# Kernel tuning notes

Measured on AMD Instinct MI355X. Metric: run time of the kernel, lower is better.

The kernel has to match this reference:

```python
import jax, jax.numpy as jnp
import numpy as np

B, T, F, H = 32, 1024, 128, 256
NUM_LAYERS = 3  # 2 return_sequences LSTMs + final LSTM


def setup_inputs() -> dict:
    key = jax.random.key(0)
    ks = jax.random.split(key, 2 + 3 * NUM_LAYERS + 2)
    x = jax.random.normal(ks[0], (B, 2, T, F), jnp.float32)
    # ragged lengths: pad tail with zeros (Masking(mask_value=0) semantics)
    lengths = jax.random.randint(ks[1], (B, 2), T // 4, T + 1)
    tmask = (jnp.arange(T)[None, None, :] < lengths[:, :, None]).astype(jnp.float32)
    x = x * tmask[..., None]
    inp = {"inputs": x}
    in_dims = [F] + [H] * (NUM_LAYERS - 1)
    for i, d in enumerate(in_dims):
        k = 2 + 3 * i
        inp[f"W{i}"] = jax.random.normal(ks[k], (d, 4 * H), jnp.float32) * (1.0 / np.sqrt(d))
        inp[f"U{i}"] = jax.random.normal(ks[k + 1], (H, 4 * H), jnp.float32) * (1.0 / np.sqrt(H))
        b = jnp.zeros((4 * H,), jnp.float32)
        inp[f"b{i}"] = b.at[H:2 * H].set(1.0)  # keras unit_forget_bias
    inp["dense_w"] = jax.random.normal(ks[-2], (1, 1), jnp.float32)
    inp["dense_b"] = jnp.zeros((1,), jnp.float32)
    return inp


def lstm_layer(x, mask, W, U, b):
    """Keras-style masked LSTM. x: [B,T,D], mask: [B,T] bool.
    Masked steps carry previous h/c and previous output (keras K.rnn masking).
    Gate order i,f,g,o; sigmoid recurrent activation, tanh activation."""
    xT = jnp.swapaxes(x, 0, 1)                  # [T,B,D]
    mT = jnp.swapaxes(mask, 0, 1)[..., None]    # [T,B,1]
    bsz, hd = x.shape[0], U.shape[0]
    h0 = jnp.zeros((bsz, hd), x.dtype)

    def step(carry, inp):
        h, c = carry
        x_t, m = inp
        z = x_t @ W + h @ U + b                 # [B,4H]
        i, f, g, o = jnp.split(z, 4, axis=-1)
        c_new = jax.nn.sigmoid(f) * c + jax.nn.sigmoid(i) * jnp.tanh(g)
        h_new = jax.nn.sigmoid(o) * jnp.tanh(c_new)
        h = jnp.where(m, h_new, h)
        c = jnp.where(m, c_new, c)
        return (h, c), h

    (h_final, _), ys = jax.lax.scan(step, (h0, h0), (xT, mT))
    return jnp.swapaxes(ys, 0, 1), h_final


def encode(x, Ws, Us, bs):
    mask = jnp.any(x != 0, axis=-1)             # Masking(mask_value=0)
    for W, U, b in zip(Ws[:-1], Us[:-1], bs[:-1]):
        x, _ = lstm_layer(x, mask, W, U, b)     # dropout is identity at inference
    _, h = lstm_layer(x, mask, Ws[-1], Us[-1], bs[-1])
    return h


def reference(inputs, W0, U0, b0, W1, U1, b1, W2, U2, b2, dense_w, dense_b):
    Ws, Us, bs = [W0, W1, W2], [U0, U1, U2], [b0, b1, b2]
    h1 = encode(inputs[:, 0], Ws, Us, bs)
    h2 = encode(inputs[:, 1], Ws, Us, bs)
    dist = jnp.linalg.norm(h1 - h2, axis=1, keepdims=True)   # [B,1]
    dist = jnp.clip(dist, 1e-7, 1e7)
    return jax.nn.sigmoid(dist @ dense_w + dense_b)          # [B,1]
```

## Files before the change

### kernel.cpp

```cpp
#include <hip/hip_runtime.h>


typedef __attribute__((ext_vector_type(8))) short bf16x8;
typedef __attribute__((ext_vector_type(4))) float f32x4;
typedef __attribute__((ext_vector_type(4))) unsigned int u32x4;
typedef unsigned long long ull;

__device__ __forceinline__ unsigned short f2bf(float f){
    unsigned u = __float_as_uint(f);
    u += 0x7FFFu + ((u >> 16) & 1u);
    return (unsigned short)(u >> 16);
}
__device__ __forceinline__ float fsig(float x){ return 1.0f / (1.0f + __expf(-x)); }
__device__ __forceinline__ float ftanh(float x){
    float e = __expf(-2.0f * fabsf(x));
    float t = (1.0f - e) / (1.0f + e);
    return copysignf(t, x);
}
__device__ __forceinline__ ull ald(const ull* p){
    return __hip_atomic_load(p, __ATOMIC_RELAXED, __HIP_MEMORY_SCOPE_AGENT);
}
__device__ __forceinline__ void ast(unsigned int* p, unsigned int v){
    __hip_atomic_store(p, v, __ATOMIC_RELAXED, __HIP_MEMORY_SCOPE_AGENT);
}
__device__ __forceinline__ int min4(ull a, ull b){
    int x0 = (int)(unsigned)a, x1 = (int)(a >> 32);
    int x2 = (int)(unsigned)b, x3 = (int)(b >> 32);
    return min(min(x0, x1), min(x2, x3));
}

#define LOAD4_SC1(P, O0,O1,O2,O3)                                        \
  asm volatile("global_load_dwordx4 %0, %4, off sc1\n\t"                 \
               "global_load_dwordx4 %1, %4, off offset:1024 sc1\n\t"     \
               "global_load_dwordx4 %2, %4, off offset:2048 sc1\n\t"     \
               "global_load_dwordx4 %3, %4, off offset:3072 sc1"         \
               : "=&v"(O0),"=&v"(O1),"=&v"(O2),"=&v"(O3)                 \
               : "v"(P) : "memory")
#define LOAD4_PLAIN(P, O0,O1,O2,O3)                                      \
  asm volatile("global_load_dwordx4 %0, %4, off\n\t"                     \
               "global_load_dwordx4 %1, %4, off offset:1024\n\t"         \
               "global_load_dwordx4 %2, %4, off offset:2048\n\t"         \
               "global_load_dwordx4 %3, %4, off offset:3072"             \
               : "=&v"(O0),"=&v"(O1),"=&v"(O2),"=&v"(O3)                 \
               : "v"(P) : "memory")

__global__ void prep_kernel(const float* __restrict__ x, unsigned int* __restrict__ xb,
                            unsigned int* __restrict__ mb, int* __restrict__ fl){
    const int s = blockIdx.x, c = blockIdx.y, l = threadIdx.x;
    if (s == 0 && c == 0){ for (int i = l; i < 256; i += 64) fl[i] = 0; }
    const int g = s >> 4, sg = s & 15;
    const int woff = ((l >> 4) * 4 + ((l >> 2) & 3)) * 64 + sg * 4 + (l & 3);
    const float* xs = x + ((size_t)s * 1024 + (size_t)c * 64) * 128;
    unsigned int w0 = 0, w1 = 0;
    for (int tt = 0; tt < 64; ++tt){
        const float2 v = *(const float2*)(xs + (size_t)tt * 128 + 2 * l);
        bool nz = (v.x != 0.0f) || (v.y != 0.0f);
        unsigned long long b = __ballot(nz);
        if (b){ if (tt < 32) w0 |= 1u << tt; else w1 |= 1u << (tt - 32); }
        unsigned int p = (unsigned)f2bf(v.x) | ((unsigned)f2bf(v.y) << 16);
        xb[((size_t)(c * 64 + tt) * 4 + g) * 1024 + woff] = p;
    }
    if (l == 0){ mb[s * 32 + c * 2] = w0; mb[s * 32 + c * 2 + 1] = w1; }
}

template<int LAYER>
__device__ __forceinline__ void scan_layer(
    const unsigned int* xin,
    unsigned int* hout,
    const float* __restrict__ W, const float* __restrict__ U, const float* __restrict__ Bv,
    const unsigned int* __restrict__ mb,
    float* __restrict__ hfinal,
    int* flags)
{
    constexpr int DK = (LAYER == 0) ? 4 : 8;
    constexpr int KT = DK + 8;
    const int bid = blockIdx.x & 15;
    const int g = bid >> 2, n = bid & 3;
    const int tid  = threadIdx.x;
    const int w    = tid >> 6;
    const int lane = tid & 63;
    const int l15  = lane & 15, lk = lane >> 4;
    const int up   = lane & 7,  s2 = lane >> 3;

    __shared__ float zw[4][16][68];
    __shared__ unsigned int mbL[16][32];
    __shared__ int sgl;
    if (tid == 0) sgl = 0;
    for (int i = tid; i < 512; i += 256)
        mbL[i >> 5][i & 31] = mb[(g * 16 + (i >> 5)) * 32 + (i & 31)];
    __syncthreads();
    if (tid < 16){
        int last = 0;
        #pragma unroll
        for (int q = 0; q < 32; ++q){
            unsigned v = mbL[tid][q];
            if (v) last = q * 32 + (32 - __clz(v));
        }
        atomicMax(&sgl, last);
    }

    float bfr[4]; int gcol[4];
    #pragma unroll
    for (int nt = 0; nt < 4; ++nt){
        int lc = w * 64 + nt * 16 + l15;
        gcol[nt] = (lc & 3) * 256 + n * 64 + (lc >> 2);
        bfr[nt] = Bv[gcol[nt]];
    }
    bf16x8 Bf[KT][4];
    #pragma unroll
    for (int kt = 0; kt < KT; ++kt){
        const float* src = (kt < DK) ? (W + (size_t)(kt * 32 + lk * 8) * 1024)
                                     : (U + (size_t)((kt - DK) * 32 + lk * 8) * 1024);
        #pragma unroll
        for (int nt = 0; nt < 4; ++nt){
            bf16x8 v;
            #pragma unroll
            for (int j = 0; j < 8; ++j) v[j] = (short)f2bf(src[(size_t)j * 1024 + gcol[nt]]);
            Bf[kt][nt] = v;
        }
    }
    __syncthreads();
    const int gl = sgl;
    int* pF  = flags + (LAYER * 4 + g) * 16;
    int* pG  = flags + ((LAYER > 0 ? LAYER - 1 : 0) * 4 + g) * 16;

    float c00 = 0, c01 = 0, c10 = 0, c11 = 0;
    float h00 = 0, h01 = 0, h10 = 0, h11 = 0;
    const int myseq0 = g * 16 + s2, myseq1 = g * 16 + s2 + 8;
    const int hcol = n * 32 + w * 8 + up;
    const int woff0 = ((hcol >> 4) * 4 + ((hcol >> 2) & 3)) * 64 + s2 * 4 + (hcol & 3);

    for (int t = 0; t < gl; ++t){
        u32x4 x0v,x1v,x2v,x3v,x4v,x5v,x6v,x7v;
        u32x4 h0v,h1v,h2v,h3v,h4v,h5v,h6v,h7v;
        if (LAYER == 0){
            ull xaddr = (ull)((const char*)(xin + ((size_t)t * 4 + g) * 1024) + lane * 16);
            LOAD4_PLAIN(xaddr, x0v, x1v, x2v, x3v);
        }
        if (LAYER > 0 || t > 0){
            const ull* f  = (const ull*)pF;
            const ull* gq = (const ull*)pG;
            int spins = 0;
            for (;;){
                bool ok = true;
                if (t > 0)           ok = (min4(ald(f),  ald(f + 1))  >= t);
                if (LAYER > 0 && ok) ok = (min4(ald(gq), ald(gq + 1)) >= t + 1);
                if (ok) break;
                if ((++spins & 63) == 0) __builtin_amdgcn_s_sleep(1);
            }
        }
        if (LAYER > 0){
            ull xaddr = (ull)((const char*)(xin + ((size_t)t * 4 + g) * 2048) + lane * 16);
            LOAD4_SC1(xaddr,        x0v, x1v, x2v, x3v);
            LOAD4_SC1(xaddr + 4096, x4v, x5v, x6v, x7v);
        }
        if (t > 0){
            size_t hb = ((size_t)(LAYER == 2 ? ((t - 1) & 7) : (t - 1)) * 4 + g) * 2048;
            ull haddr = (ull)((const char*)(hout + hb) + lane * 16);
            LOAD4_SC1(haddr,        h0v, h1v, h2v, h3v);
            LOAD4_SC1(haddr + 4096, h4v, h5v, h6v, h7v);
        }
        asm volatile("s_waitcnt vmcnt(0)" ::: "memory");
        __builtin_amdgcn_sched_barrier(0);

        bf16x8 xa[DK];
        xa[0] = __builtin_bit_cast(bf16x8, x0v); xa[1] = __builtin_bit_cast(bf16x8, x1v);
        xa[2] = __builtin_bit_cast(bf16x8, x2v); xa[3] = __builtin_bit_cast(bf16x8, x3v);
        if (LAYER > 0){
            xa[DK - 4] = __builtin_bit_cast(bf16x8, x4v); xa[DK - 3] = __builtin_bit_cast(bf16x8, x5v);
            xa[DK - 2] = __builtin_bit_cast(bf16x8, x6v); xa[DK - 1] = __builtin_bit_cast(bf16x8, x7v);
        }
        f32x4 acc[4];
        #pragma unroll
        for (int nt = 0; nt < 4; ++nt) acc[nt] = (f32x4){bfr[nt], bfr[nt], bfr[nt], bfr[nt]};
        #pragma unroll
        for (int kt = 0; kt < DK; ++kt)
            #pragma unroll
            for (int nt = 0; nt < 4; ++nt)
                acc[nt] = __builtin_amdgcn_mfma_f32_16x16x32_bf16(xa[kt], Bf[kt][nt], acc[nt], 0, 0, 0);
        if (t > 0){
            bf16x8 ha[8];
            ha[0] = __builtin_bit_cast(bf16x8, h0v); ha[1] = __builtin_bit_cast(bf16x8, h1v);
            ha[2] = __builtin_bit_cast(bf16x8, h2v); ha[3] = __builtin_bit_cast(bf16x8, h3v);
            ha[4] = __builtin_bit_cast(bf16x8, h4v); ha[5] = __builtin_bit_cast(bf16x8, h5v);
            ha[6] = __builtin_bit_cast(bf16x8, h6v); ha[7] = __builtin_bit_cast(bf16x8, h7v);
            #pragma unroll
            for (int kh = 0; kh < 8; ++kh)
                #pragma unroll
                for (int nt = 0; nt < 4; ++nt)
                    acc[nt] = __builtin_amdgcn_mfma_f32_16x16x32_bf16(ha[kh], Bf[DK + kh][nt], acc[nt], 0, 0, 0);
        }
        #pragma unroll
        for (int nt = 0; nt < 4; ++nt)
            #pragma unroll
            for (int r = 0; r < 4; ++r)
                zw[w][lk * 4 + r][nt * 16 + l15] = acc[nt][r];
        asm volatile("s_waitcnt lgkmcnt(0)" ::: "memory");
        __builtin_amdgcn_sched_barrier(0);

        bool m0 = (mbL[s2][t >> 5]     >> (t & 31)) & 1;
        bool m1 = (mbL[s2 + 8][t >> 5] >> (t & 31)) & 1;
        const float* z0 = &zw[w][s2][up * 8];
        const float* z1 = &zw[w][s2 + 8][up * 8];
        float cn, hn;
        cn = fsig(z0[1]) * c00 + fsig(z0[0]) * ftanh(z0[2]); hn = fsig(z0[3]) * ftanh(cn);
        if (m0){ c00 = cn; h00 = hn; }
        cn = fsig(z0[5]) * c01 + fsig(z0[4]) * ftanh(z0[6]); hn = fsig(z0[7]) * ftanh(cn);
        if (m0){ c01 = cn; h01 = hn; }
        cn = fsig(z1[1]) * c10 + fsig(z1[0]) * ftanh(z1[2]); hn = fsig(z1[3]) * ftanh(cn);
        if (m1){ c10 = cn; h10 = hn; }
        cn = fsig(z1[5]) * c11 + fsig(z1[4]) * ftanh(z1[6]); hn = fsig(z1[7]) * ftanh(cn);
        if (m1){ c11 = cn; h11 = hn; }

        unsigned p0 = (unsigned)f2bf(h00) | ((unsigned)f2bf(h01) << 16);
        unsigned p1 = (unsigned)f2bf(h10) | ((unsigned)f2bf(h11) << 16);
        size_t dblk = ((size_t)(LAYER == 2 ? (t & 7) : t) * 4 + g) * 2048;
        ast(hout + dblk + woff0,      p0);
        ast(hout + dblk + woff0 + 32, p1);
        asm volatile("s_waitcnt vmcnt(0)" ::: "memory");
        __syncthreads();
        if (tid == 0) ast((unsigned*)(pF + n), (unsigned)(t + 1));
    }

    if (LAYER == 2){
        const int colb = n * 64 + w * 16 + up * 2;
        hfinal[(size_t)myseq0 * 256 + colb]     = h00;
        hfinal[(size_t)myseq0 * 256 + colb + 1] = h01;
        hfinal[(size_t)myseq1 * 256 + colb]     = h10;
        hfinal[(size_t)myseq1 * 256 + colb + 1] = h11;
    }
}

__global__ __launch_bounds__(256, 1) void scan3_kernel(
    const unsigned int* xb, unsigned int* h0, unsigned int* h1, unsigned int* h2,
    const float* W0, const float* U0, const float* b0,
    const float* W1, const float* U1, const float* b1,
    const float* W2, const float* U2, const float* b2,
    const unsigned int* mb, int* flags, float* hfinal)
{
    const int layer = blockIdx.x >> 4;
    if (layer == 0)      scan_layer<0>(xb, h0, W0, U0, b0, mb, nullptr, flags);
    else if (layer == 1) scan_layer<1>(h0, h1, W1, U1, b1, mb, nullptr, flags);
    else                 scan_layer<2>(h1, h2, W2, U2, b2, mb, hfinal,  flags);
}

__global__ void final_kernel(const float* __restrict__ hfinal, const float* __restrict__ dw,
                             const float* __restrict__ db, float* __restrict__ out){
    const int b = threadIdx.x >> 3, j = threadIdx.x & 7;
    const float* ha = hfinal + (size_t)(2 * b) * 256;
    const float* hb = ha + 256;
    float s = 0.0f;
    for (int d = j; d < 256; d += 8){ float df = ha[d] - hb[d]; s += df * df; }
    #pragma unroll
    for (int off = 4; off; off >>= 1) s += __shfl_xor(s, off, 8);
    if (j == 0){
        float dist = sqrtf(s);
        dist = fminf(fmaxf(dist, 1e-7f), 1e7f);
        out[b] = fsig(dist * dw[0] + db[0]);
    }
}

extern "C" void kernel_launch(void* const* d_in, const int* in_sizes, int n_in,
                              void* d_out, int out_size, void* d_ws, size_t ws_size,
                              hipStream_t stream){
    const float* x  = (const float*)d_in[0];
    const float* W0 = (const float*)d_in[1];
    const float* U0 = (const float*)d_in[2];
    const float* b0 = (const float*)d_in[3];
    const float* W1 = (const float*)d_in[4];
    const float* U1 = (const float*)d_in[5];
    const float* b1 = (const float*)d_in[6];
    const float* W2 = (const float*)d_in[7];
    const float* U2 = (const float*)d_in[8];
    const float* b2 = (const float*)d_in[9];
    const float* dw = (const float*)d_in[10];
    const float* db = (const float*)d_in[11];

    char* ws = (char*)d_ws;
    unsigned int* xb     = (unsigned int*)(ws);
    unsigned int* h0     = (unsigned int*)(ws + 16777216ull);
    unsigned int* h1     = (unsigned int*)(ws + 50331648ull);
    unsigned int* h2     = (unsigned int*)(ws + 83886080ull);
    unsigned int* mb     = (unsigned int*)(ws + 84148224ull);
    int*          flags  = (int*)(ws + 84156416ull);
    float*        hfinal = (float*)(ws + 84157440ull);
    float*        out    = (float*)d_out;

    prep_kernel<<<dim3(64, 16), 64, 0, stream>>>(x, xb, mb, flags);
    scan3_kernel<<<48, 256, 0, stream>>>(xb, h0, h1, h2,
                                         W0, U0, b0, W1, U1, b1, W2, U2, b2,
                                         mb, flags, hfinal);
    final_kernel<<<1, 256, 0, stream>>>(hfinal, dw, db, out);
}
```

Before: 3.308 ms.

## Replace flag polling and block barrier with tagged h-ring self-validating loads

Each hidden-state word is now stored with its timestep tag in the upper 32 bits, so consumers poll the data itself until the tags match. This removes the per-step s_waitcnt, __syncthreads and flag store, and the separate flag-load spin. Layer outputs become bounded rings (128 steps, 8 for the last layer) with coarse progress counters every 32 steps for backpressure. The rings are zeroed by a memset. Per-step loads double in size because of the tag words, and correctness now depends on 64-bit store atomicity and on the ring-wrap throttling.

```diff
diff --git a/kernel.cpp b/kernel.cpp
--- a/kernel.cpp
+++ b/kernel.cpp
@@ -23,18 +23,25 @@
 __device__ __forceinline__ void ast(unsigned int* p, unsigned int v){
     __hip_atomic_store(p, v, __ATOMIC_RELAXED, __HIP_MEMORY_SCOPE_AGENT);
 }
-__device__ __forceinline__ int min4(ull a, ull b){
-    int x0 = (int)(unsigned)a, x1 = (int)(a >> 32);
-    int x2 = (int)(unsigned)b, x3 = (int)(b >> 32);
-    return min(min(x0, x1), min(x2, x3));
-}
-
-#define LOAD4_SC1(P, O0,O1,O2,O3)                                        \
+__device__ __forceinline__ void st_pair(ull* p, ull v){
+    asm volatile("global_store_dwordx2 %0, %1, off sc1" :: "v"((ull)p), "v"(v) : "memory");
+}
+__device__ __forceinline__ int min16(const ull* p){
+    int m = 0x7FFFFFFF;
+    #pragma unroll
+    for (int i = 0; i < 8; ++i){
+        ull v = ald(p + i);
+        m = min(m, min((int)(unsigned)v, (int)(v >> 32)));
+    }
+    return m;
+}
+
+#define LOADT4(P, Q0,Q1,Q2,Q3)                                           \
   asm volatile("global_load_dwordx4 %0, %4, off sc1\n\t"                 \
-               "global_load_dwordx4 %1, %4, off offset:1024 sc1\n\t"     \
+               "global_load_dwordx4 %1, %4, off offset:16 sc1\n\t"       \
                "global_load_dwordx4 %2, %4, off offset:2048 sc1\n\t"     \
-               "global_load_dwordx4 %3, %4, off offset:3072 sc1"         \
-               : "=&v"(O0),"=&v"(O1),"=&v"(O2),"=&v"(O3)                 \
+               "global_load_dwordx4 %3, %4, off offset:2064 sc1"         \
+               : "=&v"(Q0),"=&v"(Q1),"=&v"(Q2),"=&v"(Q3)                 \
                : "v"(P) : "memory")
 #define LOAD4_PLAIN(P, O0,O1,O2,O3)                                      \
   asm volatile("global_load_dwordx4 %0, %4, off\n\t"                     \
@@ -44,10 +51,20 @@
                : "=&v"(O0),"=&v"(O1),"=&v"(O2),"=&v"(O3)                 \
                : "v"(P) : "memory")
 
+__device__ __forceinline__ bool tags16(const u32x4* q, unsigned tg){
+    bool ok = true;
+    #pragma unroll
+    for (int i = 0; i < 16; ++i) ok = ok && (q[i].y == tg) && (q[i].w == tg);
+    return ok;
+}
+__device__ __forceinline__ bf16x8 frag(u32x4 q0, u32x4 q1){
+    u32x4 f = (u32x4){q0.x, q0.z, q1.x, q1.z};
+    return __builtin_bit_cast(bf16x8, f);
+}
+
 __global__ void prep_kernel(const float* __restrict__ x, unsigned int* __restrict__ xb,
-                            unsigned int* __restrict__ mb, int* __restrict__ fl){
+                            unsigned int* __restrict__ mb){
     const int s = blockIdx.x, c = blockIdx.y, l = threadIdx.x;
-    if (s == 0 && c == 0){ for (int i = l; i < 256; i += 64) fl[i] = 0; }
     const int g = s >> 4, sg = s & 15;
     const int woff = ((l >> 4) * 4 + ((l >> 2) & 3)) * 64 + sg * 4 + (l & 3);
     const float* xs = x + ((size_t)s * 1024 + (size_t)c * 64) * 128;
@@ -65,15 +82,17 @@
 
 template<int LAYER>
 __device__ __forceinline__ void scan_layer(
-    const unsigned int* xin,
-    unsigned int* hout,
+    const unsigned int* __restrict__ xb0,
+    const ull* xring,
+    ull* hring,
     const float* __restrict__ W, const float* __restrict__ U, const float* __restrict__ Bv,
     const unsigned int* __restrict__ mb,
     float* __restrict__ hfinal,
-    int* flags)
+    int* prog)
 {
     constexpr int DK = (LAYER == 0) ? 4 : 8;
     constexpr int KT = DK + 8;
+    constexpr int HM = (LAYER == 2) ? 7 : 127;
     const int bid = blockIdx.x & 15;
     const int g = bid >> 2, n = bid & 3;
     const int tid  = threadIdx.x;
@@ -121,74 +140,85 @@
     }
     __syncthreads();
     const int gl = sgl;
-    int* pF  = flags + (LAYER * 4 + g) * 16;
-    int* pG  = flags + ((LAYER > 0 ? LAYER - 1 : 0) * 4 + g) * 16;
 
     float c00 = 0, c01 = 0, c10 = 0, c11 = 0;
     float h00 = 0, h01 = 0, h10 = 0, h11 = 0;
-    const int myseq0 = g * 16 + s2, myseq1 = g * 16 + s2 + 8;
     const int hcol = n * 32 + w * 8 + up;
     const int woff0 = ((hcol >> 4) * 4 + ((hcol >> 2) & 3)) * 64 + s2 * 4 + (hcol & 3);
 
     for (int t = 0; t < gl; ++t){
-        u32x4 x0v,x1v,x2v,x3v,x4v,x5v,x6v,x7v;
-        u32x4 h0v,h1v,h2v,h3v,h4v,h5v,h6v,h7v;
+        if (LAYER > 0 && (t & 31) == 0 && lane == 0)
+            ast((unsigned*)(prog + (LAYER - 1) * 64 + g * 16 + n * 4 + w), (unsigned)t);
+        if (LAYER < 2 && (t & 31) == 0){
+            const ull* pp = (const ull*)(prog + LAYER * 64 + g * 16);
+            int spins = 0;
+            while (min16(pp) < t - 96)
+                if (((++spins) & 15) == 0) __builtin_amdgcn_s_sleep(1);
+        }
+
+        u32x4 hq[16], xq[16];
         if (LAYER == 0){
-            ull xaddr = (ull)((const char*)(xin + ((size_t)t * 4 + g) * 1024) + lane * 16);
-            LOAD4_PLAIN(xaddr, x0v, x1v, x2v, x3v);
-        }
-        if (LAYER > 0 || t > 0){
-            const ull* f  = (const ull*)pF;
-            const ull* gq = (const ull*)pG;
+            ull xaddr = (ull)((const char*)(xb0 + ((size_t)t * 4 + g) * 1024) + lane * 16);
+            LOAD4_PLAIN(xaddr, xq[0], xq[1], xq[2], xq[3]);
+        }
+        bool needH = (t > 0);
+        bool needX = (LAYER > 0);
+        if (needH || needX){
+            const ull hbB = (ull)((const char*)(hring + (((size_t)((t - 1) & HM) * 4 + g) * 2048)) + lane * 32);
+            const ull xbB = (LAYER > 0)
+                ? (ull)((const char*)(xring + (((size_t)(t & 127) * 4 + g) * 2048)) + lane * 32) : 0;
             int spins = 0;
-            for (;;){
-                bool ok = true;
-                if (t > 0)           ok = (min4(ald(f),  ald(f + 1))  >= t);
-                if (LAYER > 0 && ok) ok = (min4(ald(gq), ald(gq + 1)) >= t + 1);
-                if (ok) break;
-                if ((++spins & 63) == 0) __builtin_amdgcn_s_sleep(1);
-            }
-        }
-        if (LAYER > 0){
-            ull xaddr = (ull)((const char*)(xin + ((size_t)t * 4 + g) * 2048) + lane * 16);
-            LOAD4_SC1(xaddr,        x0v, x1v, x2v, x3v);
-            LOAD4_SC1(xaddr + 4096, x4v, x5v, x6v, x7v);
-        }
-        if (t > 0){
-            size_t hb = ((size_t)(LAYER == 2 ? ((t - 1) & 7) : (t - 1)) * 4 + g) * 2048;
-            ull haddr = (ull)((const char*)(hout + hb) + lane * 16);
-            LOAD4_SC1(haddr,        h0v, h1v, h2v, h3v);
-            LOAD4_SC1(haddr + 4096, h4v, h5v, h6v, h7v);
+            do {
+                if (needH){
+                    LOADT4(hbB,         hq[0],  hq[1],  hq[2],  hq[3]);
+                    LOADT4(hbB + 4096,  hq[4],  hq[5],  hq[6],  hq[7]);
+                    LOADT4(hbB + 8192,  hq[8],  hq[9],  hq[10], hq[11]);
+                    LOADT4(hbB + 12288, hq[12], hq[13], hq[14], hq[15]);
+                }
+                if (needX){
+                    LOADT4(xbB,         xq[0],  xq[1],  xq[2],  xq[3]);
+                    LOADT4(xbB + 4096,  xq[4],  xq[5],  xq[6],  xq[7]);
+                    LOADT4(xbB + 8192,  xq[8],  xq[9],  xq[10], xq[11]);
+                    LOADT4(xbB + 12288, xq[12], xq[13], xq[14], xq[15]);
+                }
+                asm volatile("s_waitcnt vmcnt(0)" ::: "memory");
+                __builtin_amdgcn_sched_barrier(0);
+                if (needH && __all(tags16(hq, (unsigned)t)))       needH = false;
+                if (needX && __all(tags16(xq, (unsigned)(t + 1)))) needX = false;
+                if ((needH || needX) && ((++spins & 15) == 0)) __builtin_amdgcn_s_sleep(1);
+            } while (needH || needX);
         }
         asm volatile("s_waitcnt vmcnt(0)" ::: "memory");
         __builtin_amdgcn_sched_barrier(0);
 
-        bf16x8 xa[DK];
-        xa[0] = __builtin_bit_cast(bf16x8, x0v); xa[1] = __builtin_bit_cast(bf16x8, x1v);
-        xa[2] = __builtin_bit_cast(bf16x8, x2v); xa[3] = __builtin_bit_cast(bf16x8, x3v);
-        if (LAYER > 0){
-            xa[DK - 4] = __builtin_bit_cast(bf16x8, x4v); xa[DK - 3] = __builtin_bit_cast(bf16x8, x5v);
-            xa[DK - 2] = __builtin_bit_cast(bf16x8, x6v); xa[DK - 1] = __builtin_bit_cast(bf16x8, x7v);
-        }
         f32x4 acc[4];
         #pragma unroll
         for (int nt = 0; nt < 4; ++nt) acc[nt] = (f32x4){bfr[nt], bfr[nt], bfr[nt], bfr[nt]};
-        #pragma unroll
-        for (int kt = 0; kt < DK; ++kt)
-            #pragma unroll
-            for (int nt = 0; nt < 4; ++nt)
-                acc[nt] = __builtin_amdgcn_mfma_f32_16x16x32_bf16(xa[kt], Bf[kt][nt], acc[nt], 0, 0, 0);
-        if (t > 0){
-            bf16x8 ha[8];
-            ha[0] = __builtin_bit_cast(bf16x8, h0v); ha[1] = __builtin_bit_cast(bf16x8, h1v);
-            ha[2] = __builtin_bit_cast(bf16x8, h2v); ha[3] = __builtin_bit_cast(bf16x8, h3v);
-            ha[4] = __builtin_bit_cast(bf16x8, h4v); ha[5] = __builtin_bit_cast(bf16x8, h5v);
-            ha[6] = __builtin_bit_cast(bf16x8, h6v); ha[7] = __builtin_bit_cast(bf16x8, h7v);
-            #pragma unroll
-            for (int kh = 0; kh < 8; ++kh)
+        if (LAYER == 0){
+            #pragma unroll
+            for (int kt = 0; kt < 4; ++kt){
+                bf16x8 a = __builtin_bit_cast(bf16x8, xq[kt]);
                 #pragma unroll
                 for (int nt = 0; nt < 4; ++nt)
-                    acc[nt] = __builtin_amdgcn_mfma_f32_16x16x32_bf16(ha[kh], Bf[DK + kh][nt], acc[nt], 0, 0, 0);
+                    acc[nt] = __builtin_amdgcn_mfma_f32_16x16x32_bf16(a, Bf[kt][nt], acc[nt], 0, 0, 0);
+            }
+        } else {
+            #pragma unroll
+            for (int kt = 0; kt < 8; ++kt){
+                bf16x8 a = frag(xq[2 * kt], xq[2 * kt + 1]);
+                #pragma unroll
+                for (int nt = 0; nt < 4; ++nt)
+                    acc[nt] = __builtin_amdgcn_mfma_f32_16x16x32_bf16(a, Bf[kt][nt], acc[nt], 0, 0, 0);
+            }
+        }
+        if (t > 0){
+            #pragma unroll
+            for (int kh = 0; kh < 8; ++kh){
+                bf16x8 a = frag(hq[2 * kh], hq[2 * kh + 1]);
+                #pragma unroll
+                for (int nt = 0; nt < 4; ++nt)
+                    acc[nt] = __builtin_amdgcn_mfma_f32_16x16x32_bf16(a, Bf[DK + kh][nt], acc[nt], 0, 0, 0);
+            }
         }
         #pragma unroll
         for (int nt = 0; nt < 4; ++nt)
@@ -214,16 +244,18 @@
 
         unsigned p0 = (unsigned)f2bf(h00) | ((unsigned)f2bf(h01) << 16);
         unsigned p1 = (unsigned)f2bf(h10) | ((unsigned)f2bf(h11) << 16);
-        size_t dblk = ((size_t)(LAYER == 2 ? (t & 7) : t) * 4 + g) * 2048;
-        ast(hout + dblk + woff0,      p0);
-        ast(hout + dblk + woff0 + 32, p1);
-        asm volatile("s_waitcnt vmcnt(0)" ::: "memory");
-        __syncthreads();
-        if (tid == 0) ast((unsigned*)(pF + n), (unsigned)(t + 1));
-    }
+        ull tg = ((ull)(unsigned)(t + 1)) << 32;
+        ull* dst = hring + ((size_t)(t & HM) * 4 + g) * 2048 + woff0;
+        st_pair(dst,      (ull)p0 | tg);
+        st_pair(dst + 32, (ull)p1 | tg);
+    }
+
+    if (LAYER > 0 && lane == 0)
+        ast((unsigned*)(prog + (LAYER - 1) * 64 + g * 16 + n * 4 + w), 0x40000000u);
 
     if (LAYER == 2){
         const int colb = n * 64 + w * 16 + up * 2;
+        const int myseq0 = g * 16 + s2, myseq1 = g * 16 + s2 + 8;
         hfinal[(size_t)myseq0 * 256 + colb]     = h00;
         hfinal[(size_t)myseq0 * 256 + colb + 1] = h01;
         hfinal[(size_t)myseq1 * 256 + colb]     = h10;
@@ -232,16 +264,16 @@
 }
 
 __global__ __launch_bounds__(256, 1) void scan3_kernel(
-    const unsigned int* xb, unsigned int* h0, unsigned int* h1, unsigned int* h2,
+    const unsigned int* xb, ull* h0, ull* h1, ull* h2,
     const float* W0, const float* U0, const float* b0,
     const float* W1, const float* U1, const float* b1,
     const float* W2, const float* U2, const float* b2,
-    const unsigned int* mb, int* flags, float* hfinal)
+    const unsigned int* mb, int* prog, float* hfinal)
 {
     const int layer = blockIdx.x >> 4;
-    if (layer == 0)      scan_layer<0>(xb, h0, W0, U0, b0, mb, nullptr, flags);
-    else if (layer == 1) scan_layer<1>(h0, h1, W1, U1, b1, mb, nullptr, flags);
-    else                 scan_layer<2>(h1, h2, W2, U2, b2, mb, hfinal,  flags);
+    if (layer == 0)      scan_layer<0>(xb, nullptr, h0, W0, U0, b0, mb, nullptr, prog);
+    else if (layer == 1) scan_layer<1>(nullptr, h0, h1, W1, U1, b1, mb, nullptr, prog);
+    else                 scan_layer<2>(nullptr, h1, h2, W2, U2, b2, mb, hfinal,  prog);
 }
 
 __global__ void final_kernel(const float* __restrict__ hfinal, const float* __restrict__ dw,
@@ -278,17 +310,19 @@
 
     char* ws = (char*)d_ws;
     unsigned int* xb     = (unsigned int*)(ws);
-    unsigned int* h0     = (unsigned int*)(ws + 16777216ull);
-    unsigned int* h1     = (unsigned int*)(ws + 50331648ull);
-    unsigned int* h2     = (unsigned int*)(ws + 83886080ull);
-    unsigned int* mb     = (unsigned int*)(ws + 84148224ull);
-    int*          flags  = (int*)(ws + 84156416ull);
-    float*        hfinal = (float*)(ws + 84157440ull);
+    ull*          h0     = (ull*)(ws + 16777216ull);
+    ull*          h1     = (ull*)(ws + 25165824ull);
+    ull*          h2     = (ull*)(ws + 33554432ull);
+    int*          prog   = (int*)(ws + 34078720ull);
+    unsigned int* mb     = (unsigned int*)(ws + 34079232ull);
+    float*        hfinal = (float*)(ws + 34087424ull);
     float*        out    = (float*)d_out;
 
-    prep_kernel<<<dim3(64, 16), 64, 0, stream>>>(x, xb, mb, flags);
+    (void)hipMemsetAsync(ws + 16777216ull, 0, 17302016ull, stream);
+
+    prep_kernel<<<dim3(64, 16), 64, 0, stream>>>(x, xb, mb);
     scan3_kernel<<<48, 256, 0, stream>>>(xb, h0, h1, h2,
                                          W0, U0, b0, W1, U1, b1, W2, U2, b2,
-                                         mb, flags, hfinal);
+                                         mb, prog, hfinal);
     final_kernel<<<1, 256, 0, stream>>>(hfinal, dw, db, out);
 }
```

After: 4.828 ms. 45.9% more time.
